# Kernel optimization log

Measured on AMD Instinct MI355X. Metric: run time of the kernel, lower is better.

Reference implementation:

```python
import jax, jax.numpy as jnp
import numpy as np
import math

B, N, D, K = 8, 2048, 1024, 128
PI = math.pi


def setup_inputs() -> dict:
    key = jax.random.key(0)
    ks = jax.random.split(key, 4)
    x = jax.random.normal(ks[0], (B, N, D), dtype=jnp.float32)
    W_proj = jax.random.normal(ks[1], (D, 6 * K), dtype=jnp.float32) * (D ** -0.5)
    # structured bias init as in OscillatorProjection._init_weights
    b = np.zeros(6 * K, np.float32)
    groups = [K // 4, K // 2, K - K // 4 - K // 2]
    centers = [0.3, 0.65, 0.97]
    off = 3 * K
    for n_k, c in zip(groups, centers):
        b[off:off + n_k] = math.log(c / (1.0 - c))
        off += n_k
    b[4 * K:5 * K] = math.log(0.65 / 0.35)
    b[5 * K:] = -2.0
    b_proj = jnp.asarray(b)
    omega_base = jnp.exp(jnp.linspace(math.log(2.0 * PI / N), math.log(PI * (1.0 - 1.0 / K)), K)).astype(jnp.float32)
    W_phase = jax.random.normal(ks[2], (D, K), dtype=jnp.float32) * 0.001
    b_phase = jnp.zeros((K,), jnp.float32)
    W_res = jax.random.normal(ks[3], (4 * K - 2, D), dtype=jnp.float32) * 0.002
    lambda_pcg = jnp.float32(0.5)
    res_scale = jnp.float32(0.05)
    return dict(x=x, W_proj=W_proj, b_proj=b_proj, omega_base=omega_base,
                W_phase=W_phase, b_phase=b_phase, W_res=W_res,
                lambda_pcg=lambda_pcg, res_scale=res_scale)


def _resonance_scan(alpha, drive):
    # linear recurrence r_t = alpha_t * r_{t-1} + d_t, r_0 = 0, along axis=1
    def combine(e1, e2):
        a1, b1 = e1
        a2, b2 = e2
        return (a2 * a1, a2 * b1 + b2)
    _, r = jax.lax.associative_scan(combine, (alpha, drive), axis=1)
    return r


def reference(x, W_proj, b_proj, omega_base, W_phase, b_phase, W_res, lambda_pcg, res_scale):
    _, n, _ = x.shape
    out = x @ W_proj + b_proj  # [B, n, 6K]
    A_r, Om_r, Ph_r, Ga_r, Go_r, Be_r = jnp.split(out, 6, axis=-1)
    A = jnp.minimum(jax.nn.softplus(A_r), 3.0)
    omega = jnp.clip(jax.nn.sigmoid(Om_r) * PI + omega_base, 1e-4, PI - 1e-4)
    phi = jnp.tanh(Ph_r) * PI
    alpha = jax.nn.sigmoid(Ga_r)
    g_out = jax.nn.sigmoid(Go_r)
    beta = jax.nn.sigmoid(Be_r)
    positions = jnp.log1p(jnp.arange(n, dtype=jnp.float32)).reshape(1, n, 1)
    angle = omega * positions + phi
    cos_a = jnp.cos(angle)
    sin_a = jnp.sin(angle)
    drive = (1.0 - alpha) * A
    # fused real/imag scan sharing alpha (mirrors the fused Triton path)
    r = _resonance_scan(jnp.concatenate([alpha, alpha], axis=-1),
                        jnp.concatenate([drive * cos_a, drive * sin_a], axis=-1))
    r_r, r_i = r[..., :K], r[..., K:]
    readout = r_r * cos_a + r_i * sin_a
    r_r = r_r - beta * readout * cos_a
    r_i = r_i - beta * readout * sin_a
    # state norm: rescale only when |r| > 1
    modulus = jnp.sqrt(r_r ** 2 + r_i ** 2 + 1e-8)
    scale = jnp.maximum(modulus, 1.0)
    r_r = r_r / scale
    r_i = r_i / scale
    # rotate into the oscillator frame
    rho_re = r_r * cos_a + r_i * sin_a
    rho_im = -r_r * sin_a + r_i * cos_a
    rho_norm = jnp.sqrt(rho_re ** 2 + rho_im ** 2 + 1e-6)
    pq = x @ W_phase + b_phase
    align = (rho_re * jnp.cos(pq) + rho_im * jnp.sin(pq)) / rho_norm
    gate = jax.nn.sigmoid(lambda_pcg * align)
    rho_re = gate * rho_re
    rho_im = gate * rho_im
    # SCPM: adjacent-oscillator complex cross products -> 4K-2 features
    cross_re = rho_re[..., :-1] * rho_re[..., 1:] + rho_im[..., :-1] * rho_im[..., 1:]
    cross_im = rho_im[..., :-1] * rho_re[..., 1:] - rho_re[..., :-1] * rho_im[..., 1:]
    feats = jnp.concatenate([g_out * rho_re, g_out * rho_im, cross_re, cross_im], axis=-1)
    return x + res_scale * (feats @ W_res)
```

## Files before the change

### kernel.cpp

```cpp
#include <hip/hip_runtime.h>
#include <math.h>

#define PI_F 3.14159265358979323846f
#define SEG 256
#define SLEN 8
typedef unsigned short u16;
typedef __attribute__((ext_vector_type(8))) short bf16x8;
typedef __attribute__((ext_vector_type(4))) float f32x4;

__device__ __forceinline__ float sigmoidf_(float x){ return __fdividef(1.0f, 1.0f+__expf(-x)); }
__device__ __forceinline__ float softplusf_(float x){
    return fmaxf(x, 0.f) + __logf(1.f + __expf(-fabsf(x)));
}
__device__ __forceinline__ float tanhpi_(float x){
    float t = __expf(-2.f*fabsf(x));
    float th = __fdividef(1.f - t, 1.f + t);
    return copysignf(th, x)*PI_F;
}
__device__ __forceinline__ void fsincos(float a, float* s, float* c){
    float r = a * 0.15915494309189535f;
    r = r - floorf(r);
#if __has_builtin(__builtin_amdgcn_sinf)
    *s = __builtin_amdgcn_sinf(r);
    *c = __builtin_amdgcn_cosf(r);
#else
    float t = r * 6.283185307179586f;
    *s = __sinf(t); *c = __cosf(t);
#endif
}
__device__ __forceinline__ u16 f2bf(float f){
    unsigned u = __float_as_uint(f);
    return (u16)((u + 0x7FFFu + ((u>>16)&1u)) >> 16);
}
__device__ __forceinline__ float b2f(u16 v){
    return __uint_as_float(((unsigned)v)<<16);
}
__device__ __forceinline__ void gl_lds16(const u16* g, u16* l){
    __builtin_amdgcn_global_load_lds((const __attribute__((address_space(1))) void*)g,
                                     (__attribute__((address_space(3))) void*)l, 16, 0, 0);
}

__global__ __launch_bounds__(256) void k_cvt_x(const float* __restrict__ x, u16* __restrict__ xb){
    size_t i = ((size_t)blockIdx.x*256 + threadIdx.x)*8;
    float4 v0 = *(const float4*)&x[i];
    float4 v1 = *(const float4*)&x[i+4];
    ushort4 a = make_ushort4(f2bf(v0.x),f2bf(v0.y),f2bf(v0.z),f2bf(v0.w));
    ushort4 b = make_ushort4(f2bf(v1.x),f2bf(v1.y),f2bf(v1.z),f2bf(v1.w));
    *(ushort4*)&xb[i]   = a;
    *(ushort4*)&xb[i+4] = b;
}

__global__ __launch_bounds__(256) void k_tcvt(const float* __restrict__ W, u16* __restrict__ Wt,
                                              int K, int Ns, int KD){
    __shared__ float s[32][33];
    const int tx = threadIdx.x & 31, ty = threadIdx.x >> 5;
    const int k0 = blockIdx.y*32, n0 = blockIdx.x*32;
    #pragma unroll
    for (int i=0;i<4;i++){
        int k = k0 + ty + i*8;
        s[ty+i*8][tx] = (k < K) ? W[(size_t)k*Ns + n0 + tx] : 0.f;
    }
    __syncthreads();
    #pragma unroll
    for (int i=0;i<4;i++){
        int n = n0 + ty + i*8;
        Wt[(size_t)n*KD + k0 + tx] = f2bf(s[tx][ty+i*8]);
    }
}

__global__ __launch_bounds__(256,2) void k_mm1(
    const u16* __restrict__ A,
    const u16* __restrict__ Bt,
    const float* __restrict__ bp, const float* __restrict__ bph,
    u16* __restrict__ C)
{
    __shared__ u16 sm[3*12288];
    const int bid = blockIdx.x;
    const int swz = (bid & 7)*56 + (bid >> 3);
    const int by = swz / 7, bx = swz - by*7;
    const int r0 = by*256, c0 = bx*128;
    const int tid = threadIdx.x;
    const int w = tid >> 6, lane = tid & 63;
    const int wm = w >> 1, wn = w & 1;
    const int lr = lane & 15, lk = lane >> 4;

    const int cg = ((lane&3) ^ ((lane>>3)&3))*8;
    const u16* gA = A  + (size_t)(r0 + w*16 + (lane>>2))*1024 + cg;
    const u16* gB = Bt + (size_t)(c0 + w*16 + (lane>>2))*1024 + cg;
    const int ldsA = w*512;
    const int ldsB = 8192 + w*512;

    const int cs = (lk ^ ((lr>>1)&3))*8;
    const int aoff = (wm*128 + lr)*32 + cs;
    const int boff = 8192 + (wn*64 + lr)*32 + cs;

    f32x4 acc[8][4] = {};

    #pragma unroll
    for (int t=0;t<2;t++){
        #pragma unroll
        for (int j=0;j<4;j++)
            gl_lds16(gA + j*64*1024 + t*32, sm + t*12288 + ldsA + j*2048);
        #pragma unroll
        for (int j=0;j<2;j++)
            gl_lds16(gB + j*64*1024 + t*32, sm + t*12288 + ldsB + j*2048);
    }
    asm volatile("s_waitcnt vmcnt(6)" ::: "memory");
    __builtin_amdgcn_s_barrier();
    __builtin_amdgcn_sched_barrier(0);

    for (int k=0; k<32; ++k){
        const u16* bufp = sm + (k%3)*12288;
        u16*       bufn = sm + ((k+2)%3)*12288;
        const int  k0n  = (k+2)*32;
        bf16x8 af[8], bfr[4];

        if (k < 30){
            #pragma unroll
            for (int j=0;j<4;j++)
                gl_lds16(gA + j*64*1024 + k0n, bufn + ldsA + j*2048);
            #pragma unroll
            for (int j=0;j<2;j++)
                gl_lds16(gB + j*64*1024 + k0n, bufn + ldsB + j*2048);
        }
        af[0] = *(const bf16x8*)&bufp[aoff];
        #pragma unroll
        for (int n=0;n<4;n++) bfr[n] = *(const bf16x8*)&bufp[boff + n*512];
        #pragma unroll
        for (int m=1;m<8;m++) af[m]  = *(const bf16x8*)&bufp[aoff + m*512];

        __builtin_amdgcn_s_setprio(1);
        #pragma unroll
        for (int m=0;m<8;m++)
            #pragma unroll
            for (int n=0;n<4;n++)
                acc[m][n] = __builtin_amdgcn_mfma_f32_16x16x32_bf16(af[m], bfr[n], acc[m][n],0,0,0);
        __builtin_amdgcn_s_setprio(0);

        if (k < 30)       asm volatile("s_waitcnt vmcnt(6)" ::: "memory");
        else if (k == 30) asm volatile("s_waitcnt vmcnt(0)" ::: "memory");
        __builtin_amdgcn_s_barrier();
        __builtin_amdgcn_sched_barrier(0);
    }

    #pragma unroll
    for (int n=0;n<4;n++){
        const int col = c0 + wn*64 + n*16 + lr;
        const float bl = (col < 768) ? bp[col] : bph[col-768];
        #pragma unroll
        for (int m=0;m<8;m++){
            const int row = r0 + wm*128 + m*16 + lk*4;
            #pragma unroll
            for (int r=0;r<4;r++)
                C[(size_t)(row+r)*896 + col] = f2bf(acc[m][n][r] + bl);
        }
    }
}

__global__ __launch_bounds__(256) void k_mm2(
    const u16* __restrict__ A,
    const u16* __restrict__ Bt,
    const u16* __restrict__ Xb,
    const float* __restrict__ rs_p,
    float* __restrict__ O)
{
    __shared__ u16 sm[3*8192];
    const int bid = blockIdx.x;
    const int swz = (bid & 7)*128 + (bid >> 3);
    const int by = swz >> 3, bx = swz & 7;
    const int r0 = by*128, c0 = bx*128;
    const int tid = threadIdx.x;
    const int w = tid>>6, lane = tid&63;
    const int wm = w>>1, wn = w&1;
    const int lr = lane&15, lk = lane>>4;

    const int cg = ((lane&3) ^ ((lane>>3)&3))*8;
    const u16* gA = A  + (size_t)(r0 + w*32 + (lane>>2))*512 + cg;
    const u16* gB = Bt + (size_t)(c0 + w*32 + (lane>>2))*512 + cg;
    const int ldsA = w*1024;
    const int ldsB = 4096 + w*1024;

    const int cs = (lk ^ ((lr>>1)&3))*8;
    const int aoff = (wm*64 + lr)*32 + cs;
    const int boff = 4096 + (wn*64 + lr)*32 + cs;

    f32x4 acc[4][4] = {};

    #pragma unroll
    for (int t=0;t<2;t++){
        #pragma unroll
        for (int i=0;i<2;i++){
            gl_lds16(gA + i*16*512 + t*32, sm + t*8192 + ldsA + i*512);
            gl_lds16(gB + i*16*512 + t*32, sm + t*8192 + ldsB + i*512);
        }
    }
    asm volatile("s_waitcnt vmcnt(4)" ::: "memory");
    __builtin_amdgcn_s_barrier();
    __builtin_amdgcn_sched_barrier(0);

    for (int k=0; k<16; ++k){
        const u16* bufp = sm + (k%3)*8192;
        u16*       bufn = sm + ((k+2)%3)*8192;
        const int  k0n  = (k+2)*32;
        bf16x8 af[4], bfr[4];

        if (k < 14){
            #pragma unroll
            for (int i=0;i<2;i++){
                gl_lds16(gA + i*16*512 + k0n, bufn + ldsA + i*512);
                gl_lds16(gB + i*16*512 + k0n, bufn + ldsB + i*512);
            }
        }
        af[0] = *(const bf16x8*)&bufp[aoff];
        #pragma unroll
        for (int n=0;n<4;n++) bfr[n] = *(const bf16x8*)&bufp[boff + n*512];
        #pragma unroll
        for (int m=1;m<4;m++) af[m]  = *(const bf16x8*)&bufp[aoff + m*512];

        __builtin_amdgcn_s_setprio(1);
        #pragma unroll
        for (int m=0;m<4;m++)
            #pragma unroll
            for (int n=0;n<4;n++)
                acc[m][n] = __builtin_amdgcn_mfma_f32_16x16x32_bf16(af[m], bfr[n], acc[m][n],0,0,0);
        __builtin_amdgcn_s_setprio(0);

        if (k < 14)       asm volatile("s_waitcnt vmcnt(4)" ::: "memory");
        else if (k == 14) asm volatile("s_waitcnt vmcnt(0)" ::: "memory");
        __builtin_amdgcn_s_barrier();
        __builtin_amdgcn_sched_barrier(0);
    }

    const float rs = rs_p[0];
    #pragma unroll
    for (int n=0;n<4;n++){
        int col = c0 + wn*64 + n*16 + lr;
        #pragma unroll
        for (int m=0;m<4;m++){
            int row = r0 + wm*64 + m*16 + lk*4;
            #pragma unroll
            for (int r=0;r<4;r++){
                size_t idx = (size_t)(row+r)*1024 + col;
                O[idx] = b2f(Xb[idx]) + rs*acc[m][n][r];
            }
        }
    }
}

__global__ __launch_bounds__(128) void k_s1(
    const u16* __restrict__ C1,
    const float* __restrict__ omega_base,
    float* __restrict__ Ag, float* __restrict__ Br, float* __restrict__ Bi)
{
    const int k = threadIdx.x;
    const int seg = blockIdx.x, b = blockIdx.y;
    const float ob = omega_base[k];
    const int n0 = seg*SLEN;
    float aag = 1.f, br = 0.f, bi = 0.f;
    #pragma unroll 4
    for (int s=0; s<SLEN; s++){
        const int n = n0 + s;
        const u16* row = C1 + (size_t)(b*2048+n)*896;
        float Ar = b2f(row[k]);
        float Om = b2f(row[128+k]);
        float Ph = b2f(row[256+k]);
        float Ga = b2f(row[384+k]);
        float alpha = sigmoidf_(Ga);
        float A = fminf(softplusf_(Ar), 3.0f);
        float omega = fminf(fmaxf(sigmoidf_(Om)*PI_F + ob, 1e-4f), PI_F-1e-4f);
        float phi = tanhpi_(Ph);
        float pos = __logf(1.f + (float)n);
        float sa, ca; fsincos(fmaf(omega, pos, phi), &sa, &ca);
        float drive = (1.f-alpha)*A;
        aag *= alpha;
        br = fmaf(alpha, br, drive*ca);
        bi = fmaf(alpha, bi, drive*sa);
    }
    const size_t o = (size_t)(b*SEG + seg)*128 + k;
    Ag[o] = aag; Br[o] = br; Bi[o] = bi;
}

__global__ __launch_bounds__(256) void k_s2(
    const float* __restrict__ Ag, const float* __restrict__ Br, const float* __restrict__ Bi,
    float* __restrict__ Pr, float* __restrict__ Pi)
{
    const int gid = blockIdx.x*256 + threadIdx.x;
    const int b = gid >> 7, k = gid & 127;
    float pr = 0.f, pi = 0.f;
    #pragma unroll 8
    for (int seg=0; seg<SEG; seg++){
        const size_t o = (size_t)(b*SEG + seg)*128 + k;
        float a = Ag[o], r = Br[o], i = Bi[o];
        Pr[o] = pr; Pi[o] = pi;
        pr = fmaf(a, pr, r);
        pi = fmaf(a, pi, i);
    }
}

__global__ __launch_bounds__(128) void k_s3(
    const u16* __restrict__ C1,
    const float* __restrict__ omega_base,
    const float* __restrict__ lam_p,
    const float* __restrict__ Pr, const float* __restrict__ Pi,
    u16* __restrict__ F)
{
    const int k = threadIdx.x;
    const int seg = blockIdx.x, b = blockIdx.y;
    const float ob = omega_base[k];
    const float lam = lam_p[0];
    __shared__ float sre[2][129], sim[2][129];

    const size_t po = (size_t)(b*SEG + seg)*128 + k;
    float rr = Pr[po], ri = Pi[po];
    const int n0 = seg*SLEN;

    #pragma unroll 2
    for (int s=0; s<SLEN; s++){
        const int n = n0 + s;
        const u16* row = C1 + (size_t)(b*2048+n)*896;
        float Ar = b2f(row[k]);
        float Om = b2f(row[128+k]);
        float Ph = b2f(row[256+k]);
        float Ga = b2f(row[384+k]);
        float Go = b2f(row[512+k]);
        float Be = b2f(row[640+k]);
        float pq = b2f(row[768+k]);
        float alpha = sigmoidf_(Ga);
        float A = fminf(softplusf_(Ar), 3.0f);
        float omega = fminf(fmaxf(sigmoidf_(Om)*PI_F + ob, 1e-4f), PI_F-1e-4f);
        float phi = tanhpi_(Ph);
        float pos = __logf(1.f + (float)n);
        float sa, ca; fsincos(fmaf(omega, pos, phi), &sa, &ca);
        float drive = (1.f-alpha)*A;
        rr = fmaf(alpha, rr, drive*ca);
        ri = fmaf(alpha, ri, drive*sa);
        float readout = rr*ca + ri*sa;
        float beta = sigmoidf_(Be);
        float r2r = rr - beta*readout*ca;
        float r2i = ri - beta*readout*sa;
        float m2 = r2r*r2r + r2i*r2i + 1e-8f;
        float inv = fminf(rsqrtf(m2), 1.0f);
        r2r *= inv; r2i *= inv;
        float rho_re =  r2r*ca + r2i*sa;
        float rho_im = -r2r*sa + r2i*ca;
        float rho2 = rho_re*rho_re + rho_im*rho_im + 1e-6f;
        float spq, cpq; fsincos(pq, &spq, &cpq);
        float align = (rho_re*cpq + rho_im*spq)*rsqrtf(rho2);
        float gate = sigmoidf_(lam*align);
        rho_re *= gate; rho_im *= gate;
        float go = sigmoidf_(Go);

        const int buf = s & 1;
        sre[buf][k] = rho_re; sim[buf][k] = rho_im;
        __syncthreads();

        u16* frow = F + (size_t)(b*2048+n)*512;
        frow[k]       = f2bf(go*rho_re);
        frow[128 + k] = f2bf(go*rho_im);
        if (k < 127){
            float nre = sre[buf][k+1], nim = sim[buf][k+1];
            frow[256 + k] = f2bf(rho_re*nre + rho_im*nim);
            frow[383 + k] = f2bf(rho_im*nre - rho_re*nim);
        } else {
            frow[510] = 0; frow[511] = 0;
        }
    }
}

extern "C" void kernel_launch(void* const* d_in, const int* in_sizes, int n_in,
                              void* d_out, int out_size, void* d_ws, size_t ws_size,
                              hipStream_t stream)
{
    const float* x   = (const float*)d_in[0];
    const float* Wp  = (const float*)d_in[1];
    const float* bp  = (const float*)d_in[2];
    const float* ob  = (const float*)d_in[3];
    const float* Wph = (const float*)d_in[4];
    const float* bph = (const float*)d_in[5];
    const float* Wr  = (const float*)d_in[6];
    const float* lam = (const float*)d_in[7];
    const float* rs  = (const float*)d_in[8];
    float* out = (float*)d_out;

    char* ws = (char*)d_ws;
    u16*   C1  = (u16*)  (ws + 0);
    float* Ag  = (float*)(ws + 29360128);
    float* Brr = (float*)(ws + 30408704);
    float* Bii = (float*)(ws + 31457280);
    float* Pr  = (float*)(ws + 32505856);
    float* Pi  = (float*)(ws + 33554432);
    u16*   F   = (u16*)  (ws + 34603008);
    u16*   Wt  = (u16*)  (ws + 51380224);
    u16*   Wrt = (u16*)  (ws + 53215232);
    u16*   Xb  = (u16*)  (ws + 58720256);

    dim3 blk(256);
    hipLaunchKernelGGL(k_cvt_x, dim3(8192),   blk, 0, stream, x, Xb);
    hipLaunchKernelGGL(k_tcvt,  dim3(24,32),  blk, 0, stream, Wp,  Wt,            1024, 768,  1024);
    hipLaunchKernelGGL(k_tcvt,  dim3(4,32),   blk, 0, stream, Wph, Wt + 768*1024, 1024, 128,  1024);
    hipLaunchKernelGGL(k_tcvt,  dim3(32,16),  blk, 0, stream, Wr,  Wrt,           510,  1024, 512);
    hipLaunchKernelGGL(k_mm1,   dim3(448),    blk, 0, stream, Xb, Wt, bp, bph, C1);
    hipLaunchKernelGGL(k_s1,    dim3(SEG,8),  dim3(128), 0, stream, C1, ob, Ag, Brr, Bii);
    hipLaunchKernelGGL(k_s2,    dim3(4),      blk, 0, stream, Ag, Brr, Bii, Pr, Pi);
    hipLaunchKernelGGL(k_s3,    dim3(SEG,8),  dim3(128), 0, stream, C1, ob, lam, Pr, Pi, F);
    hipLaunchKernelGGL(k_mm2,   dim3(1024),   blk, 0, stream, F, Wrt, Xb, rs, out);
}
```

Measured before the change: 132.5 us.

## Merge prep kernels and load mm1 B operand directly into registers

Folds the x conversion and the three weight transpose-convert launches into one k_prep kernel that dispatches on block index, removing three launches. In k_mm1, the B tile is no longer staged through LDS. Each wave now takes 64 rows by all 128 columns and loads its B fragments straight from global memory into double-buffered registers, while only A goes through the triple-buffered LDS pipeline. This shrinks LDS use and LDS read traffic, but every wave re-reads B from global or cache and needs more registers for the fragments.

Measured after the change: 161.8 us. 22.1% more time.

```diff
diff --git a/kernel.cpp b/kernel.cpp
--- a/kernel.cpp
+++ b/kernel.cpp
@@ -40,21 +40,31 @@
                                      (__attribute__((address_space(3))) void*)l, 16, 0, 0);
 }
 
-__global__ __launch_bounds__(256) void k_cvt_x(const float* __restrict__ x, u16* __restrict__ xb){
-    size_t i = ((size_t)blockIdx.x*256 + threadIdx.x)*8;
-    float4 v0 = *(const float4*)&x[i];
-    float4 v1 = *(const float4*)&x[i+4];
-    ushort4 a = make_ushort4(f2bf(v0.x),f2bf(v0.y),f2bf(v0.z),f2bf(v0.w));
-    ushort4 b = make_ushort4(f2bf(v1.x),f2bf(v1.y),f2bf(v1.z),f2bf(v1.w));
-    *(ushort4*)&xb[i]   = a;
-    *(ushort4*)&xb[i+4] = b;
-}
-
-__global__ __launch_bounds__(256) void k_tcvt(const float* __restrict__ W, u16* __restrict__ Wt,
-                                              int K, int Ns, int KD){
+__global__ __launch_bounds__(256) void k_prep(
+    const float* __restrict__ x,  u16* __restrict__ xb,
+    const float* __restrict__ Wp, const float* __restrict__ Wph,
+    const float* __restrict__ Wr,
+    u16* __restrict__ Wt, u16* __restrict__ Wrt)
+{
     __shared__ float s[32][33];
+    const int bid = blockIdx.x;
+    if (bid < 8192){
+        size_t i = ((size_t)bid*256 + threadIdx.x)*8;
+        float4 v0 = *(const float4*)&x[i];
+        float4 v1 = *(const float4*)&x[i+4];
+        ushort4 a = make_ushort4(f2bf(v0.x),f2bf(v0.y),f2bf(v0.z),f2bf(v0.w));
+        ushort4 b = make_ushort4(f2bf(v1.x),f2bf(v1.y),f2bf(v1.z),f2bf(v1.w));
+        *(ushort4*)&xb[i]   = a;
+        *(ushort4*)&xb[i+4] = b;
+        return;
+    }
+    int t = bid - 8192;
+    const float* W; u16* Wo; int K, Ns, KD, bx, by;
+    if (t < 768)      {           W=Wp;  Wo=Wt;            K=1024; Ns=768;  KD=1024; bx=t%24; by=t/24; }
+    else if (t < 896) { int u=t-768; W=Wph; Wo=Wt+768*1024; K=1024; Ns=128;  KD=1024; bx=u%4;  by=u/4; }
+    else              { int u=t-896; W=Wr;  Wo=Wrt;          K=510;  Ns=1024; KD=512;  bx=u%32; by=u/32; }
     const int tx = threadIdx.x & 31, ty = threadIdx.x >> 5;
-    const int k0 = blockIdx.y*32, n0 = blockIdx.x*32;
+    const int k0 = by*32, n0 = bx*32;
     #pragma unroll
     for (int i=0;i<4;i++){
         int k = k0 + ty + i*8;
@@ -64,7 +74,7 @@
     #pragma unroll
     for (int i=0;i<4;i++){
         int n = n0 + ty + i*8;
-        Wt[(size_t)n*KD + k0 + tx] = f2bf(s[tx][ty+i*8]);
+        Wo[(size_t)n*KD + k0 + tx] = f2bf(s[tx][ty+i*8]);
     }
 }
 
@@ -74,82 +84,86 @@
     const float* __restrict__ bp, const float* __restrict__ bph,
     u16* __restrict__ C)
 {
-    __shared__ u16 sm[3*12288];
+    __shared__ u16 sm[3*8192];
     const int bid = blockIdx.x;
     const int swz = (bid & 7)*56 + (bid >> 3);
     const int by = swz / 7, bx = swz - by*7;
     const int r0 = by*256, c0 = bx*128;
     const int tid = threadIdx.x;
     const int w = tid >> 6, lane = tid & 63;
-    const int wm = w >> 1, wn = w & 1;
     const int lr = lane & 15, lk = lane >> 4;
 
     const int cg = ((lane&3) ^ ((lane>>3)&3))*8;
-    const u16* gA = A  + (size_t)(r0 + w*16 + (lane>>2))*1024 + cg;
-    const u16* gB = Bt + (size_t)(c0 + w*16 + (lane>>2))*1024 + cg;
+    const u16* gA = A + (size_t)(r0 + w*16 + (lane>>2))*1024 + cg;
     const int ldsA = w*512;
-    const int ldsB = 8192 + w*512;
 
     const int cs = (lk ^ ((lr>>1)&3))*8;
-    const int aoff = (wm*128 + lr)*32 + cs;
-    const int boff = 8192 + (wn*64 + lr)*32 + cs;
-
-    f32x4 acc[8][4] = {};
-
-    #pragma unroll
-    for (int t=0;t<2;t++){
-        #pragma unroll
-        for (int j=0;j<4;j++)
-            gl_lds16(gA + j*64*1024 + t*32, sm + t*12288 + ldsA + j*2048);
-        #pragma unroll
-        for (int j=0;j<2;j++)
-            gl_lds16(gB + j*64*1024 + t*32, sm + t*12288 + ldsB + j*2048);
-    }
-    asm volatile("s_waitcnt vmcnt(6)" ::: "memory");
+    const int aoff = (w*64 + lr)*32 + cs;
+
+    const u16* gB = Bt + (size_t)(c0 + lr)*1024 + lk*8;
+
+    f32x4 acc[4][8] = {};
+    bf16x8 bfrA[8], bfrB[8];
+
+    #pragma unroll
+    for (int j=0;j<4;j++) gl_lds16(gA + j*64*1024,      sm        + ldsA + j*2048);
+    #pragma unroll
+    for (int j=0;j<4;j++) gl_lds16(gA + j*64*1024 + 32, sm + 8192 + ldsA + j*2048);
+    #pragma unroll
+    for (int n=0;n<8;n++) bfrA[n] = *(const bf16x8*)&gB[(size_t)n*16384];
+    asm volatile("s_waitcnt vmcnt(12)" ::: "memory");
     __builtin_amdgcn_s_barrier();
     __builtin_amdgcn_sched_barrier(0);
 
-    for (int k=0; k<32; ++k){
-        const u16* bufp = sm + (k%3)*12288;
-        u16*       bufn = sm + ((k+2)%3)*12288;
-        const int  k0n  = (k+2)*32;
-        bf16x8 af[8], bfr[4];
-
-        if (k < 30){
-            #pragma unroll
-            for (int j=0;j<4;j++)
-                gl_lds16(gA + j*64*1024 + k0n, bufn + ldsA + j*2048);
-            #pragma unroll
-            for (int j=0;j<2;j++)
-                gl_lds16(gB + j*64*1024 + k0n, bufn + ldsB + j*2048);
-        }
-        af[0] = *(const bf16x8*)&bufp[aoff];
-        #pragma unroll
-        for (int n=0;n<4;n++) bfr[n] = *(const bf16x8*)&bufp[boff + n*512];
-        #pragma unroll
-        for (int m=1;m<8;m++) af[m]  = *(const bf16x8*)&bufp[aoff + m*512];
-
-        __builtin_amdgcn_s_setprio(1);
-        #pragma unroll
-        for (int m=0;m<8;m++)
-            #pragma unroll
-            for (int n=0;n<4;n++)
-                acc[m][n] = __builtin_amdgcn_mfma_f32_16x16x32_bf16(af[m], bfr[n], acc[m][n],0,0,0);
-        __builtin_amdgcn_s_setprio(0);
-
-        if (k < 30)       asm volatile("s_waitcnt vmcnt(6)" ::: "memory");
-        else if (k == 30) asm volatile("s_waitcnt vmcnt(0)" ::: "memory");
-        __builtin_amdgcn_s_barrier();
-        __builtin_amdgcn_sched_barrier(0);
-    }
-
-    #pragma unroll
-    for (int n=0;n<4;n++){
-        const int col = c0 + wn*64 + n*16 + lr;
+    #define MM1_TILE(E, BCUR, BNXT)                                              \
+    {                                                                            \
+        const u16* bufp = sm + ((E)%3)*8192;                                     \
+        bf16x8 af[4];                                                            \
+        af[0] = *(const bf16x8*)&bufp[aoff];                                     \
+        af[1] = *(const bf16x8*)&bufp[aoff + 512];                               \
+        af[2] = *(const bf16x8*)&bufp[aoff + 1024];                              \
+        af[3] = *(const bf16x8*)&bufp[aoff + 1536];                              \
+        __builtin_amdgcn_s_setprio(1);                                           \
+        _Pragma("unroll")                                                        \
+        for (int m=0;m<4;m++)                                                    \
+            _Pragma("unroll")                                                    \
+            for (int n=0;n<8;n++)                                                \
+                acc[m][n] = __builtin_amdgcn_mfma_f32_16x16x32_bf16(             \
+                                af[m], BCUR[n], acc[m][n],0,0,0);                \
+        __builtin_amdgcn_s_setprio(0);                                           \
+        if ((E) < 31){                                                           \
+            _Pragma("unroll")                                                    \
+            for (int n=0;n<8;n++)                                                \
+                BNXT[n] = *(const bf16x8*)&gB[(size_t)n*16384 + ((E)+1)*32];     \
+        }                                                                        \
+        if ((E) < 30){                                                           \
+            u16* bufn = sm + (((E)+2)%3)*8192;                                   \
+            _Pragma("unroll")                                                    \
+            for (int j=0;j<4;j++)                                                \
+                gl_lds16(gA + j*64*1024 + ((E)+2)*32, bufn + ldsA + j*2048);     \
+        }                                                                        \
+        if ((E) < 30)      { asm volatile("s_waitcnt vmcnt(12)" ::: "memory");   \
+                             __builtin_amdgcn_s_barrier();                       \
+                             __builtin_amdgcn_sched_barrier(0); }                \
+        else if ((E) == 30){ asm volatile("s_waitcnt vmcnt(8)"  ::: "memory");   \
+                             __builtin_amdgcn_s_barrier();                       \
+                             __builtin_amdgcn_sched_barrier(0); }                \
+    }
+
+    for (int k2=0; k2<16; ++k2){
+        const int e0 = 2*k2, e1 = 2*k2+1;
+        MM1_TILE(e0, bfrA, bfrB)
+        MM1_TILE(e1, bfrB, bfrA)
+    }
+    #undef MM1_TILE
+
+    #pragma unroll
+    for (int n=0;n<8;n++){
+        const int col = c0 + n*16 + lr;
         const float bl = (col < 768) ? bp[col] : bph[col-768];
         #pragma unroll
-        for (int m=0;m<8;m++){
-            const int row = r0 + wm*128 + m*16 + lk*4;
+        for (int m=0;m<4;m++){
+            const int row = r0 + w*64 + m*16 + lk*4;
             #pragma unroll
             for (int r=0;r<4;r++)
                 C[(size_t)(row+r)*896 + col] = f2bf(acc[m][n][r] + bl);
@@ -395,10 +409,7 @@
     u16*   Xb  = (u16*)  (ws + 58720256);
 
     dim3 blk(256);
-    hipLaunchKernelGGL(k_cvt_x, dim3(8192),   blk, 0, stream, x, Xb);
-    hipLaunchKernelGGL(k_tcvt,  dim3(24,32),  blk, 0, stream, Wp,  Wt,            1024, 768,  1024);
-    hipLaunchKernelGGL(k_tcvt,  dim3(4,32),   blk, 0, stream, Wph, Wt + 768*1024, 1024, 128,  1024);
-    hipLaunchKernelGGL(k_tcvt,  dim3(32,16),  blk, 0, stream, Wr,  Wrt,           510,  1024, 512);
+    hipLaunchKernelGGL(k_prep,  dim3(9600),   blk, 0, stream, x, Xb, Wp, Wph, Wr, Wt, Wrt);
     hipLaunchKernelGGL(k_mm1,   dim3(448),    blk, 0, stream, Xb, Wt, bp, bph, C1);
     hipLaunchKernelGGL(k_s1,    dim3(SEG,8),  dim3(128), 0, stream, C1, ob, Ag, Brr, Bii);
     hipLaunchKernelGGL(k_s2,    dim3(4),      blk, 0, stream, Ag, Brr, Bii, Pr, Pi);
```
